# Kernel tuning notes

Hardware: AMD Instinct MI355X
Metric: run time of the kernel (lower is better)

## Reference

```python
import jax, jax.numpy as jnp
import numpy as np

LN10 = float(np.log(10.0))
EPS = 1e-10


def _band_e(L1, L2, R1, R2, rho1, rho2, g2p, g2m, gp, gm,
            cos1, sin1, cos2, sin2, epsexp, deltexp, epsdelexp):
    """EC-stage expected energy over the (tau, gamma) grid.
    L*,R*: (S,N) real; rho*: (S,N) complex -> (S, ntaus, ngammas)."""
    # first part: gamma-only terms (S,G) broadcast over taus
    first = (jnp.sum(L1 * L2, 1)[:, None] * g2p
             + jnp.sum(R1 * R2, 1)[:, None] * g2m) * epsexp
    first = first[:, None, :] + (jnp.sum(L1 * R2, 1)
                                 + jnp.sum(R1 * L2, 1))[:, None, None]
    r1r, r1i = jnp.real(rho1), jnp.imag(rho1)
    r2r, r2i = jnp.real(rho2), jnp.imag(rho2)
    # Re(rho * exp(-i*w*tau)) = Re(rho)*cos(w*tau) + Im(rho)*sin(w*tau);
    # contracting over the N frames first avoids the (S,N,ntaus) intermediate.
    sec = ((jnp.sum(L1 * r1r, 1) + jnp.sum(L2 * r2r, 1))[:, None] * cos1
           + (jnp.sum(L1 * r1i, 1) + jnp.sum(L2 * r2i, 1))[:, None] * sin1)  # (S,T)
    second = 2.0 * sec[:, :, None] * gp * epsdelexp[None]
    thr = ((jnp.sum(R1 * r1r, 1) + jnp.sum(R2 * r2r, 1))[:, None] * cos1
           + (jnp.sum(R1 * r1i, 1) + jnp.sum(R2 * r2i, 1))[:, None] * sin1)
    third = 2.0 * thr[:, :, None] * gm * epsdelexp[None]
    t1 = jnp.sum(r1r * r2r + r1i * r2i, 1)          # Re(sum rho1*conj(rho2)), (S,)
    q = jnp.sum(rho1 * rho2, 1)                     # (S,) complex
    t2 = jnp.real(q)[:, None] * cos2 + jnp.imag(q)[:, None] * sin2  # Re(q*e^{-2iwt})
    fourth = 2.0 * (t1[:, None] + deltexp[None, :] * t2)[:, :, None]
    return first - second - third + fourth


def _ec(xl_re, xl_im, xr_re, xr_im, yl_re, yl_im, yr_re, yr_im,
        cf, taus, gammas, sigma_epsilon, sigma_delta, fids, N):
    xl = xl_re + 1j * xl_im
    xr = xr_re + 1j * xr_im
    yl = yl_re + 1j * yl_im
    yr = yr_re + 1j * yr_im
    F = xl.shape[1]
    S = F - N + 1                                   # number of N-frame segments
    widx = jnp.arange(S)[:, None] + jnp.arange(N)[None, :]
    fids_np = np.asarray(fids)
    J = fids_np.shape[0]
    epsexp = jnp.exp(2.0 * LN10 ** 2 * sigma_epsilon ** 2)        # (G,)
    g2p, g2m = 10.0 ** (2.0 * gammas), 10.0 ** (-2.0 * gammas)    # (G,)
    gp, gm = 10.0 ** gammas, 10.0 ** (-gammas)
    d = []
    for i in range(J):                              # J=15 structurally distinct bands
        lo, hi = int(fids_np[i, 0]) - 1, int(fids_np[i, 1])
        c = cf[i]
        wt = c * taus
        cos1, sin1 = jnp.cos(wt), jnp.sin(wt)       # tauexp = cos - i*sin
        cos2, sin2 = jnp.cos(2.0 * wt), jnp.sin(2.0 * wt)
        deltexp = jnp.exp(-(c ** 2) * sigma_delta ** 2)           # (T,)
        epsdelexp = jnp.exp(0.5 * (LN10 ** 2 * sigma_epsilon[None, :] ** 2
                                   - (c ** 2) * sigma_delta[:, None] ** 2))  # (T,G)

        def seg(a):
            return a[lo:hi][:, widx]                # (kk,S,N) sliding windows

        def norm(s):
            L = jnp.sum(jnp.real(jnp.conj(s) * s), 0)             # (S,N)
            return L - L.mean(1, keepdims=True)

        def rho(sr, sl):
            r = jnp.sum(jnp.conj(sr) * sl, 0)                     # (S,N) complex
            return r - r.mean(1, keepdims=True)

        sxl, sxr, syl, syr = seg(xl), seg(xr), seg(yl), seg(yr)
        Lx, Rx, Ly, Ry = norm(sxl), norm(sxr), norm(syl), norm(syr)
        rhox, rhoy = rho(sxr, sxl), rho(syr, syl)
        args = (g2p, g2m, gp, gm, cos1, sin1, cos2, sin2, epsexp, deltexp, epsdelexp)
        exy = _band_e(Lx, Ly, Rx, Ry, rhoy, rhox, *args)
        exx = _band_e(Lx, Lx, Rx, Rx, rhox, rhox, *args)
        eyy = _band_e(Ly, Ly, Ry, Ry, rhoy, rhoy, *args)
        p = exy / jnp.sqrt(jnp.maximum(exx * eyy, EPS))
        d.append(jnp.max(p.reshape(S, -1), axis=1))               # max over (tau,gamma)
    return jnp.stack(d, 0)                                        # (J,S)


def setup_inputs() -> dict:
    key = jax.random.key(0)
    K, F, N, J, T, G = 128, 4000, 30, 15, 100, 40
    ks = jax.random.split(key, 8)
    names = ["xl_re", "xl_im", "xr_re", "xr_im", "yl_re", "yl_im", "yr_re", "yr_im"]
    inp = {n: 0.1 * jax.random.normal(k, (K, F), dtype=jnp.float32)
           for n, k in zip(names, ks)}
    edges = np.array([0, 3, 5, 8, 11, 15, 20, 26, 33, 41, 50, 61, 74, 89, 107, 128])
    fids = np.stack([edges[:-1] + 1, edges[1:]], axis=1).astype(np.int64)  # 1-based
    cf = 2.0 * np.pi * np.geomspace(150.0, 4000.0, J)   # centre freqs in rad/s
    taus = np.linspace(-1e-3, 1e-3, T)
    gammas = np.linspace(-1.0, 1.0, G)                  # dB/20 units
    sigma_delta = 65e-6 * (1.0 + np.abs(taus) / 1e-3)
    sigma_epsilon = np.sqrt(2.0) * (1.5 / 20.0) * (1.0 + np.abs(gammas))
    inp.update(
        cf=jnp.asarray(cf, jnp.float32),
        taus=jnp.asarray(taus, jnp.float32),
        gammas=jnp.asarray(gammas, jnp.float32),
        sigma_epsilon=jnp.asarray(sigma_epsilon, jnp.float32),
        sigma_delta=jnp.asarray(sigma_delta, jnp.float32),
        fids=jnp.asarray(fids),
        N=N,
    )
    return inp


def reference(xl_re, xl_im, xr_re, xr_im, yl_re, yl_im, yr_re, yr_im,
              cf, taus, gammas, sigma_epsilon, sigma_delta, fids, N):
    return _ec(xl_re, xl_im, xr_re, xr_im, yl_re, yl_im, yr_re, yr_im,
               cf, taus, gammas, sigma_epsilon, sigma_delta, fids, N)
```

## Files before the change

### kernel.cpp

```cpp
#include <hip/hip_runtime.h>
#include <math.h>

#define LN10_SQ 5.3018981104783984f
#define LOG2_10 3.3219280948873623f

constexpr int NWIN = 30;
constexpr int SEGS_PER_BLOCK = 64;
constexpr int NFRM = SEGS_PER_BLOCK + NWIN - 1;
constexpr int NTHREADS = 512;
constexpr int TSPLIT = 8;

__global__ __launch_bounds__(NTHREADS, 4) void ec_fused_kernel(
    const float* __restrict__ xlr, const float* __restrict__ xli,
    const float* __restrict__ xrre, const float* __restrict__ xrim,
    const float* __restrict__ ylr, const float* __restrict__ yli,
    const float* __restrict__ yrre, const float* __restrict__ yrim,
    const float* __restrict__ cf, const float* __restrict__ taus,
    const float* __restrict__ gammas, const float* __restrict__ sigeps,
    const float* __restrict__ sigdel, const int* __restrict__ fids,
    float* __restrict__ out, int F, int S, int T, int G, int K)
{
    __shared__ float4 ttabA[128];
    __shared__ float2 ttabB[128];
    __shared__ float4 gtab[64];
    __shared__ float  sser[8][96];
    __shared__ float  scal[27][64];
    __shared__ float  red[NTHREADS];

    const int tid = threadIdx.x;
    const int band = blockIdx.y;
    const int seg_base = blockIdx.x * SEGS_PER_BLOCK;
    const float cw = cf[band];

    int lo, hi;
    if (fids[1] == 0) {
        lo = fids[4 * band] - 1;
        hi = fids[4 * band + 2];
    } else {
        lo = fids[2 * band] - 1;
        hi = fids[2 * band + 1];
    }
    lo = lo < 0 ? 0 : lo;
    hi = hi > K ? K : hi;

    {
        int tt = tid - 128;
        if (tt >= 0 && tt < T) {
            float tau = taus[tt];
            float wt = cw * tau;
            float sn1, cs1, sn2, cs2;
            sincosf(wt, &sn1, &cs1);
            sincosf(2.0f * wt, &sn2, &cs2);
            float sd = sigdel[tt];
            float Dt = expf(-0.5f * cw * cw * sd * sd);
            ttabA[tt] = make_float4(cs1, sn1, cs2, sn2);
            ttabB[tt] = make_float2(2.0f * Dt, 2.0f * Dt * Dt);
        }
        int gg = tid - 256;
        if (gg >= 0 && gg < G) {
            float gam = gammas[gg];
            float se = sigeps[gg];
            float ee = expf(2.0f * LN10_SQ * se * se);
            float Eg = expf(0.5f * LN10_SQ * se * se);
            float g2p = exp2f(2.0f * gam * LOG2_10);
            float g2m = exp2f(-2.0f * gam * LOG2_10);
            float gp = exp2f(gam * LOG2_10);
            float gm = exp2f(-gam * LOG2_10);
            gtab[gg] = make_float4(g2p * ee, g2m * ee, gp * Eg, gm * Eg);
        }
    }

    if (tid < NFRM) {
        int j = tid;
        int f = seg_base + j;
        float Lx = 0.f, Rx = 0.f, Ly = 0.f, Ry = 0.f;
        float rxr = 0.f, rxi = 0.f, ryr = 0.f, ryi = 0.f;
        if (f < F) {
            for (int k = lo; k < hi; ++k) {
                int idx = k * F + f;
                float a = xlr[idx], b = xli[idx], c = xrre[idx], d = xrim[idx];
                Lx = fmaf(a, a, fmaf(b, b, Lx));
                Rx = fmaf(c, c, fmaf(d, d, Rx));
                rxr = fmaf(c, a, fmaf(d, b, rxr));
                rxi = fmaf(c, b, rxi) - d * a;
                float e = ylr[idx], g = yli[idx], h = yrre[idx], i2 = yrim[idx];
                Ly = fmaf(e, e, fmaf(g, g, Ly));
                Ry = fmaf(h, h, fmaf(i2, i2, Ry));
                ryr = fmaf(h, e, fmaf(i2, g, ryr));
                ryi = fmaf(h, g, ryi) - i2 * e;
            }
        }
        sser[0][j] = Lx;  sser[1][j] = Rx;
        sser[2][j] = Ly;  sser[3][j] = Ry;
        sser[4][j] = rxr; sser[5][j] = rxi;
        sser[6][j] = ryr; sser[7][j] = ryi;
    }
    __syncthreads();

    if (tid < SEGS_PER_BLOCK) {
        const int segL = tid;
        float s0=0,s1=0,s2=0,s3=0,s4=0,s5=0,s6=0,s7=0;
        float c00=0,c01=0,c02=0,c03=0,c04=0,c05=0,c06=0,c07=0;
        float c11=0,c12=0,c13=0,c14=0,c15=0,c16=0,c17=0;
        float c22=0,c23=0,c24=0,c25=0,c26=0,c27=0;
        float c33=0,c34=0,c35=0,c36=0,c37=0;
        float c44=0,c45=0,c46=0,c47=0;
        float c55=0,c56=0,c57=0;
        float c66=0,c67=0;
        float c77=0;
        #pragma unroll 5
        for (int n = 0; n < NWIN; ++n) {
            float v0 = sser[0][segL + n], v1 = sser[1][segL + n];
            float v2 = sser[2][segL + n], v3 = sser[3][segL + n];
            float v4 = sser[4][segL + n], v5 = sser[5][segL + n];
            float v6 = sser[6][segL + n], v7 = sser[7][segL + n];
            s0+=v0; s1+=v1; s2+=v2; s3+=v3; s4+=v4; s5+=v5; s6+=v6; s7+=v7;
            c00=fmaf(v0,v0,c00); c01=fmaf(v0,v1,c01); c02=fmaf(v0,v2,c02); c03=fmaf(v0,v3,c03);
            c04=fmaf(v0,v4,c04); c05=fmaf(v0,v5,c05); c06=fmaf(v0,v6,c06); c07=fmaf(v0,v7,c07);
            c11=fmaf(v1,v1,c11); c12=fmaf(v1,v2,c12); c13=fmaf(v1,v3,c13); c14=fmaf(v1,v4,c14);
            c15=fmaf(v1,v5,c15); c16=fmaf(v1,v6,c16); c17=fmaf(v1,v7,c17);
            c22=fmaf(v2,v2,c22); c23=fmaf(v2,v3,c23); c24=fmaf(v2,v4,c24); c25=fmaf(v2,v5,c25);
            c26=fmaf(v2,v6,c26); c27=fmaf(v2,v7,c27);
            c33=fmaf(v3,v3,c33); c34=fmaf(v3,v4,c34); c35=fmaf(v3,v5,c35); c36=fmaf(v3,v6,c36);
            c37=fmaf(v3,v7,c37);
            c44=fmaf(v4,v4,c44); c45=fmaf(v4,v5,c45); c46=fmaf(v4,v6,c46); c47=fmaf(v4,v7,c47);
            c55=fmaf(v5,v5,c55); c56=fmaf(v5,v6,c56); c57=fmaf(v5,v7,c57);
            c66=fmaf(v6,v6,c66); c67=fmaf(v6,v7,c67);
            c77=fmaf(v7,v7,c77);
        }
        const float rN = 1.0f / (float)NWIN;
        #define CEN(a,b) fmaf(-(s##a * rN), s##b, c##a##b)
        float t46 = CEN(4,6), t57 = CEN(5,7), t56 = CEN(5,6), t47 = CEN(4,7);
        scal[0][segL] = CEN(0,2);
        scal[1][segL] = CEN(1,3);
        scal[2][segL] = CEN(0,3) + CEN(1,2) + 2.0f*(t46+t57);
        scal[3][segL] = CEN(0,6) + CEN(2,4);
        scal[4][segL] = CEN(0,7) + CEN(2,5);
        scal[5][segL] = CEN(1,6) + CEN(3,4);
        scal[6][segL] = CEN(1,7) + CEN(3,5);
        scal[7][segL] = t46 - t57;
        scal[8][segL] = t56 + t47;
        float t44 = CEN(4,4), t55 = CEN(5,5);
        scal[9][segL]  = CEN(0,0);
        scal[10][segL] = CEN(1,1);
        scal[11][segL] = 2.0f*CEN(0,1) + 2.0f*(t44+t55);
        scal[12][segL] = 2.0f*CEN(0,4);
        scal[13][segL] = 2.0f*CEN(0,5);
        scal[14][segL] = 2.0f*CEN(1,4);
        scal[15][segL] = 2.0f*CEN(1,5);
        scal[16][segL] = t44 - t55;
        scal[17][segL] = 2.0f*CEN(4,5);
        float t66 = CEN(6,6), t77 = CEN(7,7);
        scal[18][segL] = CEN(2,2);
        scal[19][segL] = CEN(3,3);
        scal[20][segL] = 2.0f*CEN(2,3) + 2.0f*(t66+t77);
        scal[21][segL] = 2.0f*CEN(2,6);
        scal[22][segL] = 2.0f*CEN(2,7);
        scal[23][segL] = 2.0f*CEN(3,6);
        scal[24][segL] = 2.0f*CEN(3,7);
        scal[25][segL] = t66 - t77;
        scal[26][segL] = 2.0f*CEN(6,7);
        #undef CEN
    }
    __syncthreads();

    const int seg = tid & (SEGS_PER_BLOCK - 1);
    const int split = tid >> 6;
    float A_xy = scal[0][seg],  B_xy = scal[1][seg],  base_xy = scal[2][seg];
    float sc_xy = scal[3][seg], ss_xy = scal[4][seg];
    float tc_xy = scal[5][seg], ts_xy = scal[6][seg];
    float qr_xy = scal[7][seg], qi_xy = scal[8][seg];
    float A_xx = scal[9][seg],  B_xx = scal[10][seg], base_xx = scal[11][seg];
    float sc_xx = scal[12][seg], ss_xx = scal[13][seg];
    float tc_xx = scal[14][seg], ts_xx = scal[15][seg];
    float qr_xx = scal[16][seg], qi_xx = scal[17][seg];
    float A_yy = scal[18][seg], B_yy = scal[19][seg], base_yy = scal[20][seg];
    float sc_yy = scal[21][seg], ss_yy = scal[22][seg];
    float tc_yy = scal[23][seg], ts_yy = scal[24][seg];
    float qr_yy = scal[25][seg], qi_yy = scal[26][seg];

    asm volatile("" : "+v"(A_xy), "+v"(B_xy), "+v"(base_xy), "+v"(sc_xy),
                      "+v"(ss_xy), "+v"(tc_xy), "+v"(ts_xy), "+v"(qr_xy),
                      "+v"(qi_xy), "+v"(A_xx), "+v"(B_xx), "+v"(base_xx),
                      "+v"(sc_xx), "+v"(ss_xx), "+v"(tc_xx), "+v"(ts_xx));
    asm volatile("" : "+v"(qr_xx), "+v"(qi_xx), "+v"(A_yy), "+v"(B_yy),
                      "+v"(base_yy), "+v"(sc_yy), "+v"(ss_yy), "+v"(tc_yy),
                      "+v"(ts_yy), "+v"(qr_yy), "+v"(qi_yy));

    const int tstart = __builtin_amdgcn_readfirstlane((split * T) / TSPLIT);
    const int tend   = __builtin_amdgcn_readfirstlane(((split + 1) * T) / TSPLIT);

    float m = -3.4e38f;
    for (int t = tstart; t < tend; ++t) {
        float4 ta = ttabA[t];
        float2 tb = ttabB[t];
        float w_xy = fmaf(tb.y, fmaf(qi_xy, ta.w, qr_xy * ta.z), base_xy);
        float ud_xy = fmaf(ss_xy, ta.y, sc_xy * ta.x) * tb.x;
        float vd_xy = fmaf(ts_xy, ta.y, tc_xy * ta.x) * tb.x;
        float w_xx = fmaf(tb.y, fmaf(qi_xx, ta.w, qr_xx * ta.z), base_xx);
        float ud_xx = fmaf(ss_xx, ta.y, sc_xx * ta.x) * tb.x;
        float vd_xx = fmaf(ts_xx, ta.y, tc_xx * ta.x) * tb.x;
        float w_yy = fmaf(tb.y, fmaf(qi_yy, ta.w, qr_yy * ta.z), base_yy);
        float ud_yy = fmaf(ss_yy, ta.y, sc_yy * ta.x) * tb.x;
        float vd_yy = fmaf(ts_yy, ta.y, tc_yy * ta.x) * tb.x;
        #pragma unroll 4
        for (int g = 0; g < G; ++g) {
            float4 gt = gtab[g];
            float exy = fmaf(A_xy, gt.x, w_xy);
            exy = fmaf(B_xy, gt.y, exy);
            exy = fmaf(-ud_xy, gt.z, exy);
            exy = fmaf(-vd_xy, gt.w, exy);
            float exx = fmaf(A_xx, gt.x, w_xx);
            exx = fmaf(B_xx, gt.y, exx);
            exx = fmaf(-ud_xx, gt.z, exx);
            exx = fmaf(-vd_xx, gt.w, exx);
            float eyy = fmaf(A_yy, gt.x, w_yy);
            eyy = fmaf(B_yy, gt.y, eyy);
            eyy = fmaf(-ud_yy, gt.z, eyy);
            eyy = fmaf(-vd_yy, gt.w, eyy);
            float den = fmaxf(exx * eyy, 1e-10f);
            float p = exy * __builtin_amdgcn_rsqf(den);
            m = fmaxf(m, p);
        }
    }

    red[tid] = m;
    __syncthreads();
    if (tid < SEGS_PER_BLOCK) {
        float r = red[tid];
        #pragma unroll
        for (int kk = 1; kk < TSPLIT; ++kk)
            r = fmaxf(r, red[tid + 64 * kk]);
        int sg = seg_base + tid;
        if (sg < S) out[(size_t)band * S + sg] = r;
    }
}

extern "C" void kernel_launch(void* const* d_in, const int* in_sizes, int n_in,
                              void* d_out, int out_size, void* d_ws, size_t ws_size,
                              hipStream_t stream) {
    const float* xlr  = (const float*)d_in[0];
    const float* xli  = (const float*)d_in[1];
    const float* xrre = (const float*)d_in[2];
    const float* xrim = (const float*)d_in[3];
    const float* ylr  = (const float*)d_in[4];
    const float* yli  = (const float*)d_in[5];
    const float* yrre = (const float*)d_in[6];
    const float* yrim = (const float*)d_in[7];
    const float* cfp  = (const float*)d_in[8];
    const float* taus = (const float*)d_in[9];
    const float* gammas = (const float*)d_in[10];
    const float* sigeps = (const float*)d_in[11];
    const float* sigdel = (const float*)d_in[12];
    const int*   fids = (const int*)d_in[13];

    const int J = in_sizes[8];
    const int T = in_sizes[9];
    const int G = in_sizes[10];
    const int S = out_size / J;
    const int F = S + NWIN - 1;
    const int K = in_sizes[0] / F;

    dim3 b(NTHREADS), g((S + SEGS_PER_BLOCK - 1) / SEGS_PER_BLOCK, J);
    ec_fused_kernel<<<g, b, 0, stream>>>(xlr, xli, xrre, xrim,
                                         ylr, yli, yrre, yrim,
                                         cfp, taus, gammas, sigeps, sigdel,
                                         fids, (float*)d_out, F, S, T, G, K);
}
```

Measured before the change: 126.9 us.

## Split fused EC kernel into prep, window-stats and sweep kernels via workspace

Replaces the single fused kernel with three launches when enough workspace is available: a per-frame band-energy pass that also writes per-band tau/gamma tables, a windowed covariance pass producing the 27 per-segment coefficients, and a sweep kernel that only loads tables and coefficients before the tau-gamma max loop. The goal is to stop recomputing overlapping frame sums and tables in every block, and to free the sweep kernel from prep work and its LDS footprint. In exchange it adds two extra launches and global round-trips through the workspace. The fused kernel is kept as a fallback, with its launch bounds minimum-occupancy hint removed.

```diff
diff --git a/kernel.cpp b/kernel.cpp
--- a/kernel.cpp
+++ b/kernel.cpp
@@ -9,8 +9,256 @@
 constexpr int NFRM = SEGS_PER_BLOCK + NWIN - 1;
 constexpr int NTHREADS = 512;
 constexpr int TSPLIT = 8;
-
-__global__ __launch_bounds__(NTHREADS, 4) void ec_fused_kernel(
+constexpr int TABSTRIDE = 1024;
+constexpr int TAB_RESERVE = 16384;
+
+__global__ __launch_bounds__(256) void ec_prep(
+    const float* __restrict__ xlr, const float* __restrict__ xli,
+    const float* __restrict__ xrre, const float* __restrict__ xrim,
+    const float* __restrict__ ylr, const float* __restrict__ yli,
+    const float* __restrict__ yrre, const float* __restrict__ yrim,
+    const float* __restrict__ cf, const float* __restrict__ taus,
+    const float* __restrict__ gammas, const float* __restrict__ sigeps,
+    const float* __restrict__ sigdel, const int* __restrict__ fids,
+    float* __restrict__ ser, float* __restrict__ tab,
+    int F, int T, int G, int K)
+{
+    const int band = blockIdx.y;
+    const int tid = threadIdx.x;
+    const float cw = cf[band];
+
+    if (blockIdx.x == 0) {
+        if (tid < T) {
+            float tau = taus[tid];
+            float wt = cw * tau;
+            float sn1, cs1, sn2, cs2;
+            sincosf(wt, &sn1, &cs1);
+            sincosf(2.0f * wt, &sn2, &cs2);
+            float sd = sigdel[tid];
+            float Dt = expf(-0.5f * cw * cw * sd * sd);
+            float* pa = tab + band * TABSTRIDE + tid * 4;
+            pa[0] = cs1; pa[1] = sn1; pa[2] = cs2; pa[3] = sn2;
+            float* pb = tab + band * TABSTRIDE + 512 + tid * 2;
+            pb[0] = 2.0f * Dt; pb[1] = 2.0f * Dt * Dt;
+        }
+        int gg = tid - 128;
+        if (gg >= 0 && gg < G) {
+            float gam = gammas[gg];
+            float se = sigeps[gg];
+            float ee = expf(2.0f * LN10_SQ * se * se);
+            float Eg = expf(0.5f * LN10_SQ * se * se);
+            float* pg = tab + band * TABSTRIDE + 768 + gg * 4;
+            pg[0] = exp2f(2.0f * gam * LOG2_10) * ee;
+            pg[1] = exp2f(-2.0f * gam * LOG2_10) * ee;
+            pg[2] = exp2f(gam * LOG2_10) * Eg;
+            pg[3] = exp2f(-gam * LOG2_10) * Eg;
+        }
+    }
+
+    int lo, hi;
+    if (fids[1] == 0) { lo = fids[4 * band] - 1; hi = fids[4 * band + 2]; }
+    else              { lo = fids[2 * band] - 1; hi = fids[2 * band + 1]; }
+    lo = lo < 0 ? 0 : lo;
+    hi = hi > K ? K : hi;
+
+    const int f = blockIdx.x * 256 + tid;
+    if (f >= F) return;
+    float Lx = 0.f, Rx = 0.f, Ly = 0.f, Ry = 0.f;
+    float rxr = 0.f, rxi = 0.f, ryr = 0.f, ryi = 0.f;
+    for (int k = lo; k < hi; ++k) {
+        int idx = k * F + f;
+        float a = xlr[idx], b = xli[idx], c = xrre[idx], d = xrim[idx];
+        Lx = fmaf(a, a, fmaf(b, b, Lx));
+        Rx = fmaf(c, c, fmaf(d, d, Rx));
+        rxr = fmaf(c, a, fmaf(d, b, rxr));
+        rxi = fmaf(c, b, rxi) - d * a;
+        float e = ylr[idx], g = yli[idx], h = yrre[idx], i2 = yrim[idx];
+        Ly = fmaf(e, e, fmaf(g, g, Ly));
+        Ry = fmaf(h, h, fmaf(i2, i2, Ry));
+        ryr = fmaf(h, e, fmaf(i2, g, ryr));
+        ryi = fmaf(h, g, ryi) - i2 * e;
+    }
+    float* bs = ser + (size_t)band * 8 * F;
+    bs[0 * F + f] = Lx;  bs[1 * F + f] = Rx;
+    bs[2 * F + f] = Ly;  bs[3 * F + f] = Ry;
+    bs[4 * F + f] = rxr; bs[5 * F + f] = rxi;
+    bs[6 * F + f] = ryr; bs[7 * F + f] = ryi;
+}
+
+__global__ __launch_bounds__(256) void ec_scal(
+    const float* __restrict__ ser, float* __restrict__ scal, int F, int S)
+{
+    const int band = blockIdx.y;
+    const int seg = blockIdx.x * 256 + threadIdx.x;
+    if (seg >= S) return;
+    const float* bs = ser + (size_t)band * 8 * F;
+    float s0=0,s1=0,s2=0,s3=0,s4=0,s5=0,s6=0,s7=0;
+    float c00=0,c01=0,c02=0,c03=0,c04=0,c05=0,c06=0,c07=0;
+    float c11=0,c12=0,c13=0,c14=0,c15=0,c16=0,c17=0;
+    float c22=0,c23=0,c24=0,c25=0,c26=0,c27=0;
+    float c33=0,c34=0,c35=0,c36=0,c37=0;
+    float c44=0,c45=0,c46=0,c47=0;
+    float c55=0,c56=0,c57=0;
+    float c66=0,c67=0;
+    float c77=0;
+    #pragma unroll 5
+    for (int n = 0; n < NWIN; ++n) {
+        float v0 = bs[0*F+seg+n], v1 = bs[1*F+seg+n];
+        float v2 = bs[2*F+seg+n], v3 = bs[3*F+seg+n];
+        float v4 = bs[4*F+seg+n], v5 = bs[5*F+seg+n];
+        float v6 = bs[6*F+seg+n], v7 = bs[7*F+seg+n];
+        s0+=v0; s1+=v1; s2+=v2; s3+=v3; s4+=v4; s5+=v5; s6+=v6; s7+=v7;
+        c00=fmaf(v0,v0,c00); c01=fmaf(v0,v1,c01); c02=fmaf(v0,v2,c02); c03=fmaf(v0,v3,c03);
+        c04=fmaf(v0,v4,c04); c05=fmaf(v0,v5,c05); c06=fmaf(v0,v6,c06); c07=fmaf(v0,v7,c07);
+        c11=fmaf(v1,v1,c11); c12=fmaf(v1,v2,c12); c13=fmaf(v1,v3,c13); c14=fmaf(v1,v4,c14);
+        c15=fmaf(v1,v5,c15); c16=fmaf(v1,v6,c16); c17=fmaf(v1,v7,c17);
+        c22=fmaf(v2,v2,c22); c23=fmaf(v2,v3,c23); c24=fmaf(v2,v4,c24); c25=fmaf(v2,v5,c25);
+        c26=fmaf(v2,v6,c26); c27=fmaf(v2,v7,c27);
+        c33=fmaf(v3,v3,c33); c34=fmaf(v3,v4,c34); c35=fmaf(v3,v5,c35); c36=fmaf(v3,v6,c36);
+        c37=fmaf(v3,v7,c37);
+        c44=fmaf(v4,v4,c44); c45=fmaf(v4,v5,c45); c46=fmaf(v4,v6,c46); c47=fmaf(v4,v7,c47);
+        c55=fmaf(v5,v5,c55); c56=fmaf(v5,v6,c56); c57=fmaf(v5,v7,c57);
+        c66=fmaf(v6,v6,c66); c67=fmaf(v6,v7,c67);
+        c77=fmaf(v7,v7,c77);
+    }
+    const float rN = 1.0f / (float)NWIN;
+    #define CEN(a,b) fmaf(-(s##a * rN), s##b, c##a##b)
+    float t46 = CEN(4,6), t57 = CEN(5,7), t56 = CEN(5,6), t47 = CEN(4,7);
+    float t44 = CEN(4,4), t55 = CEN(5,5);
+    float t66 = CEN(6,6), t77 = CEN(7,7);
+    float o[27];
+    o[0]  = CEN(0,2);
+    o[1]  = CEN(1,3);
+    o[2]  = CEN(0,3) + CEN(1,2) + 2.0f*(t46+t57);
+    o[3]  = CEN(0,6) + CEN(2,4);
+    o[4]  = CEN(0,7) + CEN(2,5);
+    o[5]  = CEN(1,6) + CEN(3,4);
+    o[6]  = CEN(1,7) + CEN(3,5);
+    o[7]  = t46 - t57;
+    o[8]  = t56 + t47;
+    o[9]  = CEN(0,0);
+    o[10] = CEN(1,1);
+    o[11] = 2.0f*CEN(0,1) + 2.0f*(t44+t55);
+    o[12] = 2.0f*CEN(0,4);
+    o[13] = 2.0f*CEN(0,5);
+    o[14] = 2.0f*CEN(1,4);
+    o[15] = 2.0f*CEN(1,5);
+    o[16] = t44 - t55;
+    o[17] = 2.0f*CEN(4,5);
+    o[18] = CEN(2,2);
+    o[19] = CEN(3,3);
+    o[20] = 2.0f*CEN(2,3) + 2.0f*(t66+t77);
+    o[21] = 2.0f*CEN(2,6);
+    o[22] = 2.0f*CEN(2,7);
+    o[23] = 2.0f*CEN(3,6);
+    o[24] = 2.0f*CEN(3,7);
+    o[25] = t66 - t77;
+    o[26] = 2.0f*CEN(6,7);
+    #undef CEN
+    #pragma unroll
+    for (int c = 0; c < 27; ++c)
+        scal[((size_t)band * 27 + c) * S + seg] = o[c];
+}
+
+__global__ __launch_bounds__(NTHREADS) void ec_sweep(
+    const float* __restrict__ tab, const float* __restrict__ scal,
+    float* __restrict__ out, int S, int T, int G)
+{
+    __shared__ float4 ltaA[128];
+    __shared__ float2 ltaB[128];
+    __shared__ float4 lgt[64];
+    __shared__ float  red[NTHREADS];
+
+    const int tid = threadIdx.x;
+    const int band = blockIdx.y;
+    const int seg_base = blockIdx.x * SEGS_PER_BLOCK;
+    const float* tb = tab + band * TABSTRIDE;
+
+    if (tid < 128) {
+        if (tid < T) ltaA[tid] = ((const float4*)tb)[tid];
+    } else if (tid < 256) {
+        int tt = tid - 128;
+        if (tt < T) ltaB[tt] = ((const float2*)(tb + 512))[tt];
+    } else if (tid < 320) {
+        int gg = tid - 256;
+        if (gg < G) lgt[gg] = ((const float4*)(tb + 768))[gg];
+    }
+    __syncthreads();
+
+    const int seg = seg_base + (tid & 63);
+    const int segc = seg < S ? seg : S - 1;
+    const float* sp = scal + (size_t)band * 27 * S + segc;
+    float A_xy  = sp[0*S],  B_xy  = sp[1*S],  base_xy = sp[2*S];
+    float sc_xy = sp[3*S],  ss_xy = sp[4*S];
+    float tc_xy = sp[5*S],  ts_xy = sp[6*S];
+    float qr_xy = sp[7*S],  qi_xy = sp[8*S];
+    float A_xx  = sp[9*S],  B_xx  = sp[10*S], base_xx = sp[11*S];
+    float sc_xx = sp[12*S], ss_xx = sp[13*S];
+    float tc_xx = sp[14*S], ts_xx = sp[15*S];
+    float qr_xx = sp[16*S], qi_xx = sp[17*S];
+    float A_yy  = sp[18*S], B_yy  = sp[19*S], base_yy = sp[20*S];
+    float sc_yy = sp[21*S], ss_yy = sp[22*S];
+    float tc_yy = sp[23*S], ts_yy = sp[24*S];
+    float qr_yy = sp[25*S], qi_yy = sp[26*S];
+
+    asm volatile("" : "+v"(A_xy), "+v"(B_xy), "+v"(base_xy), "+v"(sc_xy),
+                      "+v"(ss_xy), "+v"(tc_xy), "+v"(ts_xy), "+v"(qr_xy),
+                      "+v"(qi_xy), "+v"(A_xx), "+v"(B_xx), "+v"(base_xx),
+                      "+v"(sc_xx), "+v"(ss_xx), "+v"(tc_xx), "+v"(ts_xx));
+    asm volatile("" : "+v"(qr_xx), "+v"(qi_xx), "+v"(A_yy), "+v"(B_yy),
+                      "+v"(base_yy), "+v"(sc_yy), "+v"(ss_yy), "+v"(tc_yy),
+                      "+v"(ts_yy), "+v"(qr_yy), "+v"(qi_yy));
+
+    const int split = tid >> 6;
+    const int t0 = __builtin_amdgcn_readfirstlane((split * T) / TSPLIT);
+    const int t1 = __builtin_amdgcn_readfirstlane(((split + 1) * T) / TSPLIT);
+
+    float m = -3.4e38f;
+    for (int t = t0; t < t1; ++t) {
+        float4 ta = ltaA[t];
+        float2 tv = ltaB[t];
+        float w1 = fmaf(tv.y, fmaf(qi_xy, ta.w, qr_xy * ta.z), base_xy);
+        float u1 = fmaf(ss_xy, ta.y, sc_xy * ta.x) * tv.x;
+        float v1 = fmaf(ts_xy, ta.y, tc_xy * ta.x) * tv.x;
+        float w2 = fmaf(tv.y, fmaf(qi_xx, ta.w, qr_xx * ta.z), base_xx);
+        float u2 = fmaf(ss_xx, ta.y, sc_xx * ta.x) * tv.x;
+        float v2 = fmaf(ts_xx, ta.y, tc_xx * ta.x) * tv.x;
+        float w3 = fmaf(tv.y, fmaf(qi_yy, ta.w, qr_yy * ta.z), base_yy);
+        float u3 = fmaf(ss_yy, ta.y, sc_yy * ta.x) * tv.x;
+        float v3 = fmaf(ts_yy, ta.y, tc_yy * ta.x) * tv.x;
+        #pragma unroll 4
+        for (int g = 0; g < G; ++g) {
+            float4 gt = lgt[g];
+            float exy = fmaf(A_xy, gt.x, w1);
+            exy = fmaf(B_xy, gt.y, exy);
+            exy = fmaf(-u1, gt.z, exy);
+            exy = fmaf(-v1, gt.w, exy);
+            float exx = fmaf(A_xx, gt.x, w2);
+            exx = fmaf(B_xx, gt.y, exx);
+            exx = fmaf(-u2, gt.z, exx);
+            exx = fmaf(-v2, gt.w, exx);
+            float eyy = fmaf(A_yy, gt.x, w3);
+            eyy = fmaf(B_yy, gt.y, eyy);
+            eyy = fmaf(-u3, gt.z, eyy);
+            eyy = fmaf(-v3, gt.w, eyy);
+            float den = fmaxf(exx * eyy, 1e-10f);
+            m = fmaxf(m, exy * __builtin_amdgcn_rsqf(den));
+        }
+    }
+
+    red[tid] = m;
+    __syncthreads();
+    if (tid < SEGS_PER_BLOCK) {
+        float r = red[tid];
+        #pragma unroll
+        for (int kk = 1; kk < TSPLIT; ++kk)
+            r = fmaxf(r, red[tid + 64 * kk]);
+        int sg = seg_base + tid;
+        if (sg < S) out[(size_t)band * S + sg] = r;
+    }
+}
+
+__global__ __launch_bounds__(NTHREADS) void ec_fused_kernel(
     const float* __restrict__ xlr, const float* __restrict__ xli,
     const float* __restrict__ xrre, const float* __restrict__ xrim,
     const float* __restrict__ ylr, const float* __restrict__ yli,
@@ -33,13 +281,8 @@
     const float cw = cf[band];
 
     int lo, hi;
-    if (fids[1] == 0) {
-        lo = fids[4 * band] - 1;
-        hi = fids[4 * band + 2];
-    } else {
-        lo = fids[2 * band] - 1;
-        hi = fids[2 * band + 1];
-    }
+    if (fids[1] == 0) { lo = fids[4 * band] - 1; hi = fids[4 * band + 2]; }
+    else              { lo = fids[2 * band] - 1; hi = fids[2 * band + 1]; }
     lo = lo < 0 ? 0 : lo;
     hi = hi > K ? K : hi;
 
@@ -62,11 +305,8 @@
             float se = sigeps[gg];
             float ee = expf(2.0f * LN10_SQ * se * se);
             float Eg = expf(0.5f * LN10_SQ * se * se);
-            float g2p = exp2f(2.0f * gam * LOG2_10);
-            float g2m = exp2f(-2.0f * gam * LOG2_10);
-            float gp = exp2f(gam * LOG2_10);
-            float gm = exp2f(-gam * LOG2_10);
-            gtab[gg] = make_float4(g2p * ee, g2m * ee, gp * Eg, gm * Eg);
+            gtab[gg] = make_float4(exp2f(2.0f*gam*LOG2_10)*ee, exp2f(-2.0f*gam*LOG2_10)*ee,
+                                   exp2f(gam*LOG2_10)*Eg, exp2f(-gam*LOG2_10)*Eg);
         }
     }
 
@@ -187,40 +427,39 @@
                       "+v"(base_yy), "+v"(sc_yy), "+v"(ss_yy), "+v"(tc_yy),
                       "+v"(ts_yy), "+v"(qr_yy), "+v"(qi_yy));
 
-    const int tstart = __builtin_amdgcn_readfirstlane((split * T) / TSPLIT);
-    const int tend   = __builtin_amdgcn_readfirstlane(((split + 1) * T) / TSPLIT);
+    const int t0 = __builtin_amdgcn_readfirstlane((split * T) / TSPLIT);
+    const int t1 = __builtin_amdgcn_readfirstlane(((split + 1) * T) / TSPLIT);
 
     float m = -3.4e38f;
-    for (int t = tstart; t < tend; ++t) {
+    for (int t = t0; t < t1; ++t) {
         float4 ta = ttabA[t];
-        float2 tb = ttabB[t];
-        float w_xy = fmaf(tb.y, fmaf(qi_xy, ta.w, qr_xy * ta.z), base_xy);
-        float ud_xy = fmaf(ss_xy, ta.y, sc_xy * ta.x) * tb.x;
-        float vd_xy = fmaf(ts_xy, ta.y, tc_xy * ta.x) * tb.x;
-        float w_xx = fmaf(tb.y, fmaf(qi_xx, ta.w, qr_xx * ta.z), base_xx);
-        float ud_xx = fmaf(ss_xx, ta.y, sc_xx * ta.x) * tb.x;
-        float vd_xx = fmaf(ts_xx, ta.y, tc_xx * ta.x) * tb.x;
-        float w_yy = fmaf(tb.y, fmaf(qi_yy, ta.w, qr_yy * ta.z), base_yy);
-        float ud_yy = fmaf(ss_yy, ta.y, sc_yy * ta.x) * tb.x;
-        float vd_yy = fmaf(ts_yy, ta.y, tc_yy * ta.x) * tb.x;
+        float2 tv = ttabB[t];
+        float w1 = fmaf(tv.y, fmaf(qi_xy, ta.w, qr_xy * ta.z), base_xy);
+        float u1 = fmaf(ss_xy, ta.y, sc_xy * ta.x) * tv.x;
+        float v1 = fmaf(ts_xy, ta.y, tc_xy * ta.x) * tv.x;
+        float w2 = fmaf(tv.y, fmaf(qi_xx, ta.w, qr_xx * ta.z), base_xx);
+        float u2 = fmaf(ss_xx, ta.y, sc_xx * ta.x) * tv.x;
+        float v2 = fmaf(ts_xx, ta.y, tc_xx * ta.x) * tv.x;
+        float w3 = fmaf(tv.y, fmaf(qi_yy, ta.w, qr_yy * ta.z), base_yy);
+        float u3 = fmaf(ss_yy, ta.y, sc_yy * ta.x) * tv.x;
+        float v3 = fmaf(ts_yy, ta.y, tc_yy * ta.x) * tv.x;
         #pragma unroll 4
         for (int g = 0; g < G; ++g) {
             float4 gt = gtab[g];
-            float exy = fmaf(A_xy, gt.x, w_xy);
+            float exy = fmaf(A_xy, gt.x, w1);
             exy = fmaf(B_xy, gt.y, exy);
-            exy = fmaf(-ud_xy, gt.z, exy);
-            exy = fmaf(-vd_xy, gt.w, exy);
-            float exx = fmaf(A_xx, gt.x, w_xx);
+            exy = fmaf(-u1, gt.z, exy);
+            exy = fmaf(-v1, gt.w, exy);
+            float exx = fmaf(A_xx, gt.x, w2);
             exx = fmaf(B_xx, gt.y, exx);
-            exx = fmaf(-ud_xx, gt.z, exx);
-            exx = fmaf(-vd_xx, gt.w, exx);
-            float eyy = fmaf(A_yy, gt.x, w_yy);
+            exx = fmaf(-u2, gt.z, exx);
+            exx = fmaf(-v2, gt.w, exx);
+            float eyy = fmaf(A_yy, gt.x, w3);
             eyy = fmaf(B_yy, gt.y, eyy);
-            eyy = fmaf(-ud_yy, gt.z, eyy);
-            eyy = fmaf(-vd_yy, gt.w, eyy);
+            eyy = fmaf(-u3, gt.z, eyy);
+            eyy = fmaf(-v3, gt.w, eyy);
             float den = fmaxf(exx * eyy, 1e-10f);
-            float p = exy * __builtin_amdgcn_rsqf(den);
-            m = fmaxf(m, p);
+            m = fmaxf(m, exy * __builtin_amdgcn_rsqf(den));
         }
     }
 
@@ -261,9 +500,26 @@
     const int F = S + NWIN - 1;
     const int K = in_sizes[0] / F;
 
-    dim3 b(NTHREADS), g((S + SEGS_PER_BLOCK - 1) / SEGS_PER_BLOCK, J);
-    ec_fused_kernel<<<g, b, 0, stream>>>(xlr, xli, xrre, xrim,
-                                         ylr, yli, yrre, yrim,
-                                         cfp, taus, gammas, sigeps, sigdel,
-                                         fids, (float*)d_out, F, S, T, G, K);
+    const size_t ser_f  = (size_t)J * 8 * F;
+    const size_t scal_f = (size_t)J * 27 * S;
+    const size_t need   = (TAB_RESERVE + ser_f + scal_f) * sizeof(float);
+
+    if (ws_size >= need) {
+        float* tab  = (float*)d_ws;
+        float* ser  = tab + TAB_RESERVE;
+        float* scal = ser + ser_f;
+        dim3 b1(256), g1((F + 255) / 256, J);
+        ec_prep<<<g1, b1, 0, stream>>>(xlr, xli, xrre, xrim, ylr, yli, yrre, yrim,
+                                       cfp, taus, gammas, sigeps, sigdel, fids,
+                                       ser, tab, F, T, G, K);
+        dim3 b2(256), g2((S + 255) / 256, J);
+        ec_scal<<<g2, b2, 0, stream>>>(ser, scal, F, S);
+        dim3 b3(NTHREADS), g3((S + SEGS_PER_BLOCK - 1) / SEGS_PER_BLOCK, J);
+        ec_sweep<<<g3, b3, 0, stream>>>(tab, scal, (float*)d_out, S, T, G);
+    } else {
+        dim3 b(NTHREADS), g((S + SEGS_PER_BLOCK - 1) / SEGS_PER_BLOCK, J);
+        ec_fused_kernel<<<g, b, 0, stream>>>(xlr, xli, xrre, xrim, ylr, yli, yrre, yrim,
+                                             cfp, taus, gammas, sigeps, sigdel,
+                                             fids, (float*)d_out, F, S, T, G, K);
+    }
 }
```

Result: slower. 131.3 us (+3.5%).
